# Optimization experiments

Hardware: AMD Instinct MI355X
Metric: run time of the kernel (lower is better)

## Reference

```python
import jax, jax.numpy as jnp
import numpy as np

V, E, H, S, B, T = 32000, 256, 512, 128, 32, 32


def setup_inputs() -> dict:
    key = jax.random.key(0)
    ks = iter(jax.random.split(key, 32))

    def w(shape, s=0.05):
        return jax.random.normal(next(ks), shape, dtype=jnp.float32) * s

    return dict(
        src=jax.random.randint(next(ks), (S, B), 0, V),
        trg=jax.random.randint(next(ks), (T, B), 0, V),
        embed=w((V, E)),
        enc_Wih_f=w((4 * H, E)), enc_Whh_f=w((4 * H, H)), enc_bih_f=w((4 * H,)), enc_bhh_f=w((4 * H,)),
        enc_Wih_b=w((4 * H, E)), enc_Whh_b=w((4 * H, H)), enc_bih_b=w((4 * H,)), enc_bhh_b=w((4 * H,)),
        attn_W=w((H, 2 * H)), attn_b=w((H,)), attn_v=w((H,)),
        dec_Wih0=w((4 * H, H + E)), dec_Whh0=w((4 * H, H)), dec_bih0=w((4 * H,)), dec_bhh0=w((4 * H,)),
        dec_Wih1=w((4 * H, H)), dec_Whh1=w((4 * H, H)), dec_bih1=w((4 * H,)), dec_bhh1=w((4 * H,)),
        out_W=w((V, 2 * H)), out_b=w((V,)),
    )


def _cell(x, h, c, Wih, Whh, bih, bhh):
    # PyTorch LSTM gate order: i, f, g, o
    z = x @ Wih.T + h @ Whh.T + bih + bhh
    i, f, g, o = jnp.split(z, 4, axis=-1)
    c2 = jax.nn.sigmoid(f) * c + jax.nn.sigmoid(i) * jnp.tanh(g)
    h2 = jax.nn.sigmoid(o) * jnp.tanh(c2)
    return h2, c2


def _run_lstm(xs, Wih, Whh, bih, bhh):
    # xs: [S, B, in]; returns outputs [S,B,H], final (h,c)
    h0 = jnp.zeros((xs.shape[1], Whh.shape[1]), xs.dtype)

    def step(carry, x):
        h, c = carry
        h2, c2 = _cell(x, h, c, Wih, Whh, bih, bhh)
        return (h2, c2), h2

    (hT, cT), outs = jax.lax.scan(step, (h0, h0), xs)
    return outs, hT, cT


def _forward(src, trg, embed,
             enc_Wih_f, enc_Whh_f, enc_bih_f, enc_bhh_f,
             enc_Wih_b, enc_Whh_b, enc_bih_b, enc_bhh_b,
             attn_W, attn_b, attn_v,
             dec_Wih0, dec_Whh0, dec_bih0, dec_bhh0,
             dec_Wih1, dec_Whh1, dec_bih1, dec_bhh1,
             out_W, out_b):
    emb_src = embed[src]                                  # [S,B,E]
    # bidirectional 1-layer encoder LSTM
    f_outs, hf, cf = _run_lstm(emb_src, enc_Wih_f, enc_Whh_f, enc_bih_f, enc_bhh_f)
    b_outs, hb, cb = _run_lstm(emb_src[::-1], enc_Wih_b, enc_Whh_b, enc_bih_b, enc_bhh_b)
    enc_out = f_outs + b_outs[::-1]                       # [S,B,H] (sum of directions)
    h = jnp.stack([hf, hb])                               # [2,B,H] -> decoder init state
    c = jnp.stack([cf, cb])
    enc_bsh = enc_out.transpose(1, 0, 2)                  # [B,S,H]

    def dec_step(carry, tok):
        h, c = carry
        emb = embed[tok]                                  # [B,E]
        q = h[-1]                                         # top-layer hidden [B,H]
        qs = jnp.broadcast_to(q[:, None, :], enc_bsh.shape)
        energy = jnp.tanh(jnp.concatenate([qs, enc_bsh], -1) @ attn_W.T + attn_b)  # [B,S,H]
        scores = energy @ attn_v                          # [B,S]
        aw = jax.nn.softmax(scores, axis=1)
        ctx = jnp.einsum('bs,bsh->bh', aw, enc_bsh)       # [B,H]
        x = jnp.concatenate([emb, ctx], -1)               # [B,E+H]
        h0, c0 = _cell(x, h[0], c[0], dec_Wih0, dec_Whh0, dec_bih0, dec_bhh0)
        h1, c1 = _cell(h0, h[1], c[1], dec_Wih1, dec_Whh1, dec_bih1, dec_bhh1)
        logits = jax.nn.log_softmax(
            jnp.concatenate([h1, ctx], -1) @ out_W.T + out_b, axis=-1)             # [B,V]
        return (jnp.stack([h0, h1]), jnp.stack([c0, c1])), logits

    # teacher forcing (ratio=1.0): input at step t is trg[t-1]
    _, outs = jax.lax.scan(dec_step, (h, c), trg[:-1])    # [T-1,B,V]
    outputs = jnp.concatenate(
        [jnp.zeros((1,) + outs.shape[1:], outs.dtype), outs], 0)  # outputs[0]=0 as in torch
    return outputs


def reference(src, trg, embed,
              enc_Wih_f, enc_Whh_f, enc_bih_f, enc_bhh_f,
              enc_Wih_b, enc_Whh_b, enc_bih_b, enc_bhh_b,
              attn_W, attn_b, attn_v,
              dec_Wih0, dec_Whh0, dec_bih0, dec_bhh0,
              dec_Wih1, dec_Whh1, dec_bih1, dec_bhh1,
              out_W, out_b):
    return _forward(src, trg, embed,
                    enc_Wih_f, enc_Whh_f, enc_bih_f, enc_bhh_f,
                    enc_Wih_b, enc_Whh_b, enc_bih_b, enc_bhh_b,
                    attn_W, attn_b, attn_v,
                    dec_Wih0, dec_Whh0, dec_bih0, dec_bhh0,
                    dec_Wih1, dec_Whh1, dec_bih1, dec_bhh1,
                    out_W, out_b)
```

## Files before the change

### kernel.cpp

```cpp
#include <hip/hip_runtime.h>
#include <stdint.h>


using short8 = __attribute__((ext_vector_type(8))) short;
using f32x4  = __attribute__((ext_vector_type(4))) float;
typedef _Float16 half2v __attribute__((ext_vector_type(2)));

__device__ __forceinline__ short f2bf(float x){
  unsigned u = __float_as_uint(x);
  unsigned r = (u + 0x7fffu + ((u >> 16) & 1u)) >> 16;
  return (short)(unsigned short)r;
}
__device__ __forceinline__ float bf2f_lo(unsigned u){ return __uint_as_float(u << 16); }
__device__ __forceinline__ float bf2f_hi(unsigned u){ return __uint_as_float(u & 0xffff0000u); }
__device__ __forceinline__ float sigmf(float x){ return 1.0f/(1.0f + __expf(-x)); }
__device__ __forceinline__ float fast_tanh(float x){
  const float e = __expf(2.0f*x);
  return 1.0f - 2.0f/(e + 1.0f);
}
__device__ __forceinline__ unsigned pack_h2(float a, float b){
  unsigned short ha = __builtin_bit_cast(unsigned short, (_Float16)a);
  unsigned short hb = __builtin_bit_cast(unsigned short, (_Float16)b);
  return (unsigned)ha | ((unsigned)hb << 16);
}
__device__ __forceinline__ float dot2u(unsigned x, unsigned w, float c){
#if __has_builtin(__builtin_amdgcn_fdot2)
  return __builtin_amdgcn_fdot2(__builtin_bit_cast(half2v,x), __builtin_bit_cast(half2v,w), c, false);
#else
  half2v hx = __builtin_bit_cast(half2v,x), hw = __builtin_bit_cast(half2v,w);
  c = fmaf((float)hx[0], (float)hw[0], c);
  c = fmaf((float)hx[1], (float)hw[1], c);
  return c;
#endif
}

__device__ __forceinline__ float4 load_coh_f4(const float* p){
  float4 v;
  asm volatile("global_load_dwordx4 %0, %1, off sc0 sc1\n\ts_waitcnt vmcnt(0)"
               : "=&v"(v) : "v"(p) : "memory");
  return v;
}
__device__ __forceinline__ uint4 load_coh_u4(const unsigned* p){
  uint4 v;
  asm volatile("global_load_dwordx4 %0, %1, off sc0 sc1\n\ts_waitcnt vmcnt(0)"
               : "=&v"(v) : "v"(p) : "memory");
  return v;
}
__device__ __forceinline__ void load_coh_f4x4(const float* p0, const float* p1,
                                              const float* p2, const float* p3, float4* d){
  asm volatile(
    "global_load_dwordx4 %0, %4, off sc0 sc1\n\t"
    "global_load_dwordx4 %1, %5, off sc0 sc1\n\t"
    "global_load_dwordx4 %2, %6, off sc0 sc1\n\t"
    "global_load_dwordx4 %3, %7, off sc0 sc1\n\t"
    "s_waitcnt vmcnt(0)"
    : "=&v"(d[0]),"=&v"(d[1]),"=&v"(d[2]),"=&v"(d[3])
    : "v"(p0),"v"(p1),"v"(p2),"v"(p3)
    : "memory");
}
__device__ __forceinline__ void store_coh_f32(float* p, float v){
  asm volatile("global_store_dword %0, %1, off sc0 sc1" :: "v"(p), "v"(v) : "memory");
}
__device__ __forceinline__ void store_coh_u32(unsigned* p, unsigned v){
  asm volatile("global_store_dword %0, %1, off sc0 sc1" :: "v"(p), "v"(v) : "memory");
}

__device__ __forceinline__ void wait_flags(const unsigned* base, int quads, unsigned target){
  if (threadIdx.x < 64){
    const unsigned* p = base + ((threadIdx.x & (quads-1)) << 2);
    for(;;){
      uint4 v = load_coh_u4(p);
      if (__all(v.x>=target && v.y>=target && v.z>=target && v.w>=target)) break;
    }
  }
  __syncthreads();
}
__device__ __forceinline__ void set_flag(unsigned* slot, unsigned val){
  asm volatile("s_waitcnt vmcnt(0)" ::: "memory");
  __syncthreads();
  if (threadIdx.x == 0) store_coh_u32(slot, val);
}

__device__ __forceinline__ void stage8b(const float* src, unsigned* lds, int ldl){
  const int tid = threadIdx.x;
  const int row0 = tid >> 7;
  const int k4 = tid & 127;
  const float* p0 = src + (size_t)(row0    )*512 + (k4<<2);
  const float* p1 = src + (size_t)(row0 + 2)*512 + (k4<<2);
  const float* p2 = src + (size_t)(row0 + 4)*512 + (k4<<2);
  const float* p3 = src + (size_t)(row0 + 6)*512 + (k4<<2);
  float4 v[4];
  load_coh_f4x4(p0, p1, p2, p3, v);
  #pragma unroll
  for (int i = 0; i < 4; ++i){
    const int row = row0 + 2*i;
    lds[row*ldl + (k4<<1)]     = pack_h2(v[i].x, v[i].y);
    lds[row*ldl + (k4<<1) + 1] = pack_h2(v[i].z, v[i].w);
  }
}

__device__ __forceinline__ float dot512(const unsigned* xrow, const unsigned* w){
  float a = 0.f;
  #pragma unroll 4
  for (int it = 0; it < 16; ++it){
    uint4 x0 = *(const uint4*)(xrow + it*16);
    uint4 x1 = *(const uint4*)(xrow + it*16 + 4);
    uint4 x2 = *(const uint4*)(xrow + it*16 + 8);
    uint4 x3 = *(const uint4*)(xrow + it*16 + 12);
    uint4 w0 = *(const uint4*)(w + it*16);
    uint4 w1 = *(const uint4*)(w + it*16 + 4);
    uint4 w2 = *(const uint4*)(w + it*16 + 8);
    uint4 w3 = *(const uint4*)(w + it*16 + 12);
    a = dot2u(x0.x,w0.x,a); a = dot2u(x0.y,w0.y,a); a = dot2u(x0.z,w0.z,a); a = dot2u(x0.w,w0.w,a);
    a = dot2u(x1.x,w1.x,a); a = dot2u(x1.y,w1.y,a); a = dot2u(x1.z,w1.z,a); a = dot2u(x1.w,w1.w,a);
    a = dot2u(x2.x,w2.x,a); a = dot2u(x2.y,w2.y,a); a = dot2u(x2.z,w2.z,a); a = dot2u(x2.w,w2.w,a);
    a = dot2u(x3.x,w3.x,a); a = dot2u(x3.y,w3.y,a); a = dot2u(x3.z,w3.z,a); a = dot2u(x3.w,w3.w,a);
  }
  return a;
}

__device__ __forceinline__ float2 dot2rows(const unsigned* xrow, const unsigned* wA, const unsigned* wB){
  float a = 0.f, b = 0.f;
  #pragma unroll 8
  for (int it = 0; it < 32; ++it){
    uint4 x0 = *(const uint4*)(xrow + it*8);
    uint4 x1 = *(const uint4*)(xrow + it*8 + 4);
    uint4 a0 = *(const uint4*)(wA + it*8);
    uint4 a1 = *(const uint4*)(wA + it*8 + 4);
    uint4 b0 = *(const uint4*)(wB + it*8);
    uint4 b1 = *(const uint4*)(wB + it*8 + 4);
    a = dot2u(x0.x,a0.x,a); a = dot2u(x0.y,a0.y,a); a = dot2u(x0.z,a0.z,a); a = dot2u(x0.w,a0.w,a);
    a = dot2u(x1.x,a1.x,a); a = dot2u(x1.y,a1.y,a); a = dot2u(x1.z,a1.z,a); a = dot2u(x1.w,a1.w,a);
    b = dot2u(x0.x,b0.x,b); b = dot2u(x0.y,b0.y,b); b = dot2u(x0.z,b0.z,b); b = dot2u(x0.w,b0.w,b);
    b = dot2u(x1.x,b1.x,b); b = dot2u(x1.y,b1.y,b); b = dot2u(x1.w,b1.w,b); b = dot2u(x1.z,b1.z,b);
  }
  return make_float2(a, b);
}

__global__ void k_zero(float* __restrict__ p, int n){
  int i = blockIdx.x*256 + threadIdx.x;
  const int stride = gridDim.x*256;
  for (; i < n; i += stride) p[i] = 0.f;
}

__global__ __launch_bounds__(256) void k_cvt_f16(const float* __restrict__ s, unsigned short* __restrict__ d, int n){
  int i = blockIdx.x*256 + threadIdx.x;
  const int stride = gridDim.x*256;
  for (; i < n; i += stride) d[i] = __builtin_bit_cast(unsigned short, (_Float16)s[i]);
}
__global__ __launch_bounds__(256) void k_cvt_f16_str(const float* __restrict__ s, int lds_, unsigned short* __restrict__ d, int n){
  int i = blockIdx.x*256 + threadIdx.x;
  const int stride = gridDim.x*256;
  for (; i < n; i += stride){
    const int row = i >> 9, c = i & 511;
    d[i] = __builtin_bit_cast(unsigned short, (_Float16)s[(size_t)row*lds_ + c]);
  }
}

__global__ __launch_bounds__(256) void k_gather(
    const int* __restrict__ src, const int* __restrict__ trg,
    const float* __restrict__ embed,
    short* __restrict__ emb_src_bf, short* __restrict__ emb_trg_bf)
{
  const int row = blockIdx.x, tid = threadIdx.x;
  if (row < 4096){
    const int tok = src[row];
    emb_src_bf[(size_t)row*256 + tid] = f2bf(embed[(size_t)tok*256 + tid]);
  } else {
    const int r = row - 4096;
    short v = 0;
    if (r < 992){ const int tok = trg[r]; v = f2bf(embed[(size_t)tok*256 + tid]); }
    emb_trg_bf[(size_t)r*256 + tid] = v;
  }
}

__global__ __launch_bounds__(256) void k_gemm_aw(
    const short* __restrict__ A, int lda,
    const float* __restrict__ W, int ldw,
    float* __restrict__ C, int ldc,
    const float* __restrict__ bias0, const float* __restrict__ bias1,
    int Mvalid, int K, int tmode, short* __restrict__ Cbf)
{
  __shared__ __align__(16) short As[128*32];
  __shared__ __align__(16) short Bs[128*32];
  const int tid = threadIdx.x;
  const int bm = blockIdx.x, bn = blockIdx.y;
  const int w  = tid >> 6,  l  = tid & 63;
  const int wm = w >> 1,    wn = w & 1;
  const int lr = l & 15,    lk = l >> 4;

  const int r0 = tid >> 2;
  const int s0 = (tid & 3) << 3;
  const int r1 = r0 + 64;

  const short* a0 = A + (size_t)(bm*128 + r0)*lda + s0;
  const short* a1 = A + (size_t)(bm*128 + r1)*lda + s0;
  const float* w0 = W + (size_t)(bn*128 + r0)*ldw + s0;
  const float* w1 = W + (size_t)(bn*128 + r1)*ldw + s0;

  const f32x4 zero4 = {0.f,0.f,0.f,0.f};
  f32x4 acc[4][4];
  #pragma unroll
  for (int mi=0;mi<4;mi++){
    #pragma unroll
    for (int ni=0;ni<4;ni++) acc[mi][ni] = zero4;
  }

  for (int k0 = 0; k0 < K; k0 += 32){
    short8 va0 = *(const short8*)(a0 + k0);
    short8 va1 = *(const short8*)(a1 + k0);
    float4 f00 = *(const float4*)(w0 + k0);
    float4 f01 = *(const float4*)(w0 + k0 + 4);
    float4 f10 = *(const float4*)(w1 + k0);
    float4 f11 = *(const float4*)(w1 + k0 + 4);
    short8 vb0, vb1;
    vb0[0]=f2bf(f00.x); vb0[1]=f2bf(f00.y); vb0[2]=f2bf(f00.z); vb0[3]=f2bf(f00.w);
    vb0[4]=f2bf(f01.x); vb0[5]=f2bf(f01.y); vb0[6]=f2bf(f01.z); vb0[7]=f2bf(f01.w);
    vb1[0]=f2bf(f10.x); vb1[1]=f2bf(f10.y); vb1[2]=f2bf(f10.z); vb1[3]=f2bf(f10.w);
    vb1[4]=f2bf(f11.x); vb1[5]=f2bf(f11.y); vb1[6]=f2bf(f11.z); vb1[7]=f2bf(f11.w);

    __syncthreads();
    *((short8*)As + tid)       = va0;
    *((short8*)As + tid + 256) = va1;
    *((short8*)Bs + tid)       = vb0;
    *((short8*)Bs + tid + 256) = vb1;
    __syncthreads();

    short8 af[4], bfr[4];
    #pragma unroll
    for (int mi=0;mi<4;mi++) af[mi]  = *(const short8*)&As[(wm*64 + mi*16 + lr)*32 + (lk<<3)];
    #pragma unroll
    for (int ni=0;ni<4;ni++) bfr[ni] = *(const short8*)&Bs[(wn*64 + ni*16 + lr)*32 + (lk<<3)];
    #pragma unroll
    for (int mi=0;mi<4;mi++){
      #pragma unroll
      for (int ni=0;ni<4;ni++)
        acc[mi][ni] = __builtin_amdgcn_mfma_f32_16x16x32_bf16(af[mi], bfr[ni], acc[mi][ni], 0,0,0);
    }
  }

  #pragma unroll
  for (int mi=0;mi<4;mi++){
    const int rb = bm*128 + wm*64 + mi*16 + (lk<<2);
    #pragma unroll
    for (int ni=0;ni<4;ni++){
      const int col = bn*128 + wn*64 + ni*16 + lr;
      float bv = 0.f;
      if (bias0) bv += bias0[col];
      if (bias1) bv += bias1[col];
      #pragma unroll
      for (int rr=0;rr<4;rr++){
        const int row = rb + rr;
        if (row < Mvalid){
          const float vv = acc[mi][ni][rr] + bv;
          if (Cbf)        Cbf[(size_t)row*ldc + col] = f2bf(vv);
          else if (tmode) C[(size_t)(row>>5)*65536 + (size_t)col*32 + (row&31)] = vv;
          else            C[(size_t)row*ldc + col] = vv;
        }
      }
    }
  }
}

__global__ __launch_bounds__(256,1) void k_enc_persist(
    const float* __restrict__ pre_f, const float* __restrict__ pre_b,
    const unsigned short* __restrict__ WhF, const unsigned short* __restrict__ WhB,
    float* __restrict__ f_outs, float* __restrict__ b_outs,
    float* __restrict__ c_f_out, float* __restrict__ c_b_out,
    unsigned* __restrict__ flagF, unsigned* __restrict__ flagB)
{
  __shared__ __align__(16) unsigned x_lds[8*264];
  __shared__ float zbuf[64*8];
  const int bid = blockIdx.x, tid = threadIdx.x;
  const int x = bid & 7, m = bid >> 3;
  const int dir = m & 1, bg = (m >> 1) & 3, q = m >> 3;
  const int jb = x*4 + q;
  const float* pre = dir ? pre_b : pre_f;
  const unsigned* Wh = (const unsigned*)(dir ? WhB : WhF);
  float* outs = dir ? b_outs : f_outs;
  float* c_out = dir ? c_b_out : c_f_out;
  unsigned* flags = dir ? flagB : flagF;
  const int fid = jb + 32*bg;

  const int bb = tid & 7, rr = tid >> 3;
  const int g = rr >> 3, op = rr & 7;
  const unsigned* wA = Wh + (size_t)(g*512 + jb*16 + 2*op)*256;
  const unsigned* wB = wA + 256;

  const int fo = tid & 15, fb = tid >> 4;
  const int b_out = bg*8 + fb, k_out = jb*16 + fo;
  float c_reg = 0.f;

  for (int t = 0; t < 128; ++t){
    float pz[4];
    if (tid < 128){
      const int tt = dir ? (127 - t) : t;
      const float* pt = pre + (size_t)tt*65536;
      #pragma unroll
      for (int gg = 0; gg < 4; ++gg)
        pz[gg] = pt[(size_t)(gg*512 + k_out)*32 + b_out];
    }
    if (t) wait_flags(flags + 32*bg, 8, (unsigned)t);
    if (t == 0){
      for (int i = tid; i < 8*264; i += 256) x_lds[i] = 0;
    } else {
      stage8b(outs + (size_t)(t-1)*16384 + (size_t)(bg*8)*512, x_lds, 264);
    }
    __syncthreads();

    const float2 d = dot2rows(x_lds + bb*264, wA, wB);
    zbuf[(g*16 + 2*op)*8 + bb]   = d.x;
    zbuf[(g*16 + 2*op+1)*8 + bb] = d.y;
    __syncthreads();

    if (tid < 128){
      float z[4];
      #pragma unroll
      for (int gg = 0; gg < 4; ++gg)
        z[gg] = pz[gg] + zbuf[(gg*16 + fo)*8 + fb];
      const float cn = sigmf(z[1])*c_reg + sigmf(z[0])*fast_tanh(z[2]);
      c_reg = cn;
      store_coh_f32(outs + (size_t)t*16384 + (size_t)b_out*512 + k_out, sigmf(z[3])*fast_tanh(cn));
    }
    set_flag(flags + fid, (unsigned)(t+1));
  }
  if (tid < 128) c_out[b_out*512 + k_out] = c_reg;
}

__global__ __launch_bounds__(256) void k_sum_enc(
    const float* __restrict__ f_outs, const float* __restrict__ b_outs,
    short* __restrict__ enc_sum_bf)
{
  const int i = blockIdx.x*256 + threadIdx.x;
  const int s = i >> 14, rem = i & 16383;
  enc_sum_bf[i] = f2bf(f_outs[i] + b_outs[(size_t)(127 - s)*16384 + rem]);
}

__global__ __launch_bounds__(256,1) void k_dec_persist(
    const float* __restrict__ demb,
    const unsigned short* __restrict__ Wih0h,
    const unsigned short* __restrict__ Whh0h,
    const unsigned short* __restrict__ Wih1h,
    const unsigned short* __restrict__ Whh1h,
    const float* __restrict__ bih1, const float* __restrict__ bhh1,
    const unsigned short* __restrict__ wqh,
    const float* __restrict__ attnV,
    const short* __restrict__ enc_proj_bf,
    const short* __restrict__ enc_sum_bf,
    const float* __restrict__ h0_init, const float* __restrict__ h1_init,
    const float* __restrict__ c0_init, const float* __restrict__ c1_init,
    float* __restrict__ h0buf, float* __restrict__ h1buf,
    float* __restrict__ ctxb,
    float* __restrict__ qsb,
    short* __restrict__ h1ctx,
    unsigned* __restrict__ dflag)
{
  __shared__ __align__(16) unsigned x0s[8*260];
  __shared__ __align__(16) unsigned x1s[8*260];
  __shared__ float zfin[32*9];
  __shared__ __align__(16) float q_s[512], v_s[512];
  __shared__ float part[256], aw[128], red[128];

  const int bid = blockIdx.x, tid = threadIdx.x;
  const int jb = (bid & 7)*8 + ((bid >> 3) >> 2);
  const int bg = (bid >> 3) & 3;
  const int fid = bg*64 + jb;
  unsigned* gq = dflag + bg*64;

  const int b = tid & 7, r = tid >> 3;
  const int g = r >> 3, o = r & 7;
  const int j_row = g*512 + jb*8 + o;

  const int fo = tid & 7, fb = tid >> 3;
  const int b_out = bg*8 + fb, k_out = jb*8 + fo;

  const unsigned* Wh0row = (const unsigned*)Whh0h + (size_t)j_row*256;
  const unsigned* Wh1row = (const unsigned*)Whh1h + (size_t)j_row*256;
  const unsigned* Wi0row = (const unsigned*)Wih0h + (size_t)j_row*256;
  const unsigned* Wi1row = (const unsigned*)Wih1h + (size_t)j_row*256;
  const unsigned* Wqrow  = (const unsigned*)wqh  + (size_t)(jb*8 + b)*256;

  float c0_reg = 0.f, c1_reg = 0.f, bias1g[4];
  if (tid < 64){
    c0_reg = c0_init[b_out*512 + k_out];
    c1_reg = c1_init[b_out*512 + k_out];
    #pragma unroll
    for (int gg=0; gg<4; ++gg) bias1g[gg] = bih1[gg*512 + k_out] + bhh1[gg*512 + k_out];
  }
  if (bid < 32 && tid < 128) ((float4*)v_s)[tid] = ((const float4*)attnV)[tid];

  float zh0 = 0.f;

  for (int t = 0; t < 31; ++t){
    const float demb_v = demb[(size_t)t*65536 + (size_t)j_row*32 + bg*8 + b];

    if (t){
      wait_flags(gq, 16, (unsigned)(4*t));
      stage8b(h1buf + (size_t)(t&1)*16384 + (size_t)(bg*8)*512, x1s, 260);
    } else {
      stage8b(h0_init + (size_t)(bg*8)*512, x0s, 260);
      stage8b(h1_init + (size_t)(bg*8)*512, x1s, 260);
    }
    __syncthreads();
    if (t == 0) zh0 = dot512(x0s + b*260, Wh0row);
    const float zh1 = dot512(x1s + b*260, Wh1row);
    if (tid < 64){
      const float qv = dot512(x1s + (tid>>3)*260, Wqrow);
      store_coh_f32(qsb + (size_t)(bg*8 + (tid>>3))*512 + jb*8 + b, qv);
    }

    if (bid < 32){
      set_flag(dflag + fid, (unsigned)(4*t+1));
      wait_flags(gq, 16, (unsigned)(4*t+1));
      const int ab = bid;
      if (tid < 128) ((float4*)q_s)[tid] = load_coh_f4(qsb + (size_t)ab*512 + (tid<<2));
      __syncthreads();
      {
        const int s = tid >> 1, half = tid & 1;
        const unsigned* ep = (const unsigned*)(enc_proj_bf + ((size_t)(s*32 + ab))*512 + (half << 8));
        const float* qh = q_s + (half << 8);
        const float* vh = v_s + (half << 8);
        float p = 0.f;
        for (int kk = 0; kk < 128; kk += 4){
          uint4 e = *(const uint4*)(ep + kk);
          const int k2 = kk << 1;
          p += fast_tanh(qh[k2+0] + bf2f_lo(e.x)) * vh[k2+0];
          p += fast_tanh(qh[k2+1] + bf2f_hi(e.x)) * vh[k2+1];
          p += fast_tanh(qh[k2+2] + bf2f_lo(e.y)) * vh[k2+2];
          p += fast_tanh(qh[k2+3] + bf2f_hi(e.y)) * vh[k2+3];
          p += fast_tanh(qh[k2+4] + bf2f_lo(e.z)) * vh[k2+4];
          p += fast_tanh(qh[k2+5] + bf2f_hi(e.z)) * vh[k2+5];
          p += fast_tanh(qh[k2+6] + bf2f_lo(e.w)) * vh[k2+6];
          p += fast_tanh(qh[k2+7] + bf2f_hi(e.w)) * vh[k2+7];
        }
        part[tid] = p;
      }
      __syncthreads();
      if (tid < 128){ const float sc = part[2*tid] + part[2*tid+1]; aw[tid] = sc; red[tid] = sc; }
      __syncthreads();
      for (int off = 64; off > 0; off >>= 1){
        if (tid < off) red[tid] = fmaxf(red[tid], red[tid+off]);
        __syncthreads();
      }
      const float mx = red[0];
      __syncthreads();
      if (tid < 128){ const float e = __expf(aw[tid] - mx); aw[tid] = e; red[tid] = e; }
      __syncthreads();
      for (int off = 64; off > 0; off >>= 1){
        if (tid < off) red[tid] += red[tid+off];
        __syncthreads();
      }
      const float inv = 1.0f / red[0];
      if (tid < 128) aw[tid] *= inv;
      __syncthreads();
      {
        const int cc = tid << 1;
        float x0 = 0.f, x1 = 0.f;
        for (int s2 = 0; s2 < 128; ++s2){
          const unsigned u = *(const unsigned*)(enc_sum_bf + ((size_t)(s2*32 + ab))*512 + cc);
          const float a = aw[s2];
          x0 = fmaf(a, bf2f_lo(u), x0);
          x1 = fmaf(a, bf2f_hi(u), x1);
        }
        store_coh_f32(ctxb + ab*512 + cc,     x0);
        store_coh_f32(ctxb + ab*512 + cc + 1, x1);
        h1ctx[(size_t)t*32768 + ab*1024 + 512 + cc]     = f2bf(x0);
        h1ctx[(size_t)t*32768 + ab*1024 + 512 + cc + 1] = f2bf(x1);
      }
      set_flag(dflag + fid, (unsigned)(4*t+2));
    } else {
      set_flag(dflag + fid, (unsigned)(4*t+2));
    }

    wait_flags(gq, 16, (unsigned)(4*t+2));
    stage8b(ctxb + (size_t)(bg*8)*512, x0s, 260);
    __syncthreads();
    {
      const float z = demb_v + dot512(x0s + b*260, Wi0row) + zh0;
      zfin[r*9 + b] = z;
    }
    __syncthreads();
    if (tid < 64){
      float z[4];
      #pragma unroll
      for (int gg=0; gg<4; ++gg) z[gg] = zfin[(gg*8 + fo)*9 + fb];
      const float cn = sigmf(z[1])*c0_reg + sigmf(z[0])*fast_tanh(z[2]);
      c0_reg = cn;
      store_coh_f32(h0buf + (size_t)((t+1)&1)*16384 + (size_t)b_out*512 + k_out,
                    sigmf(z[3])*fast_tanh(cn));
    }
    set_flag(dflag + fid, (unsigned)(4*t+3));

    wait_flags(gq, 16, (unsigned)(4*t+3));
    stage8b(h0buf + (size_t)((t+1)&1)*16384 + (size_t)(bg*8)*512, x1s, 260);
    __syncthreads();
    {
      const float z = dot512(x1s + b*260, Wi1row) + zh1;
      zh0 = dot512(x1s + b*260, Wh0row);
      zfin[r*9 + b] = z;
    }
    __syncthreads();
    if (tid < 64){
      float z[4];
      #pragma unroll
      for (int gg=0; gg<4; ++gg) z[gg] = bias1g[gg] + zfin[(gg*8 + fo)*9 + fb];
      const float cn = sigmf(z[1])*c1_reg + sigmf(z[0])*fast_tanh(z[2]);
      c1_reg = cn;
      const float hn = sigmf(z[3])*fast_tanh(cn);
      store_coh_f32(h1buf + (size_t)((t+1)&1)*16384 + (size_t)b_out*512 + k_out, hn);
      h1ctx[(size_t)t*32768 + (size_t)b_out*1024 + k_out] = f2bf(hn);
    }
    set_flag(dflag + fid, (unsigned)(4*t+4));
  }
}

__global__ __launch_bounds__(256) void k_logsm(float* __restrict__ out){
  float* row = out + (size_t)blockIdx.x * 32000;
  const int tid = threadIdx.x;
  __shared__ float red[256];
  float m = -3.4e38f;
  for (int i = tid; i < 32000; i += 256) m = fmaxf(m, row[i]);
  red[tid] = m; __syncthreads();
  for (int off = 128; off > 0; off >>= 1){
    if (tid < off) red[tid] = fmaxf(red[tid], red[tid+off]);
    __syncthreads();
  }
  m = red[0]; __syncthreads();
  float s = 0.f;
  for (int i = tid; i < 32000; i += 256) s += __expf(row[i] - m);
  red[tid] = s; __syncthreads();
  for (int off = 128; off > 0; off >>= 1){
    if (tid < off) red[tid] += red[tid+off];
    __syncthreads();
  }
  const float lse = m + __logf(red[0]);
  for (int i = tid; i < 32000; i += 256) row[i] -= lse;
}

extern "C" void kernel_launch(void* const* d_in, const int* in_sizes, int n_in,
                              void* d_out, int out_size, void* d_ws, size_t ws_size,
                              hipStream_t stream)
{
  (void)in_sizes; (void)n_in; (void)out_size; (void)ws_size;
  const int*   src   = (const int*)d_in[0];
  const int*   trg   = (const int*)d_in[1];
  const float* embed = (const float*)d_in[2];
  const float* eWihF = (const float*)d_in[3];
  const float* eWhhF = (const float*)d_in[4];
  const float* ebihF = (const float*)d_in[5];
  const float* ebhhF = (const float*)d_in[6];
  const float* eWihB = (const float*)d_in[7];
  const float* eWhhB = (const float*)d_in[8];
  const float* ebihB = (const float*)d_in[9];
  const float* ebhhB = (const float*)d_in[10];
  const float* attnW = (const float*)d_in[11];
  const float* attnB = (const float*)d_in[12];
  const float* attnV = (const float*)d_in[13];
  const float* dWih0 = (const float*)d_in[14];
  const float* dWhh0 = (const float*)d_in[15];
  const float* dbih0 = (const float*)d_in[16];
  const float* dbhh0 = (const float*)d_in[17];
  const float* dWih1 = (const float*)d_in[18];
  const float* dWhh1 = (const float*)d_in[19];
  const float* dbih1 = (const float*)d_in[20];
  const float* dbhh1 = (const float*)d_in[21];
  const float* outW  = (const float*)d_in[22];
  const float* outB  = (const float*)d_in[23];

  float* out = (float*)d_out;
  float* enc_in_f = out;
  float* enc_in_b = out + 8388608;
  short* enc_proj_bf = (short*)(out + 18874368);
  float* f_outs   = out + 20971520;
  float* b_outs   = out + 23068672;
  float* demb     = out + 25165824;
  short* emb_src_bf = (short*)(out + 27262976);
  short* emb_trg_bf = (short*)(out + 27787264);
  short* enc_sum_bf = (short*)(out + 27918336);
  unsigned short* wqh    = (unsigned short*)(out + 28966912);
  unsigned short* whhF_h = (unsigned short*)(out + 29229056);
  unsigned short* whhB_h = (unsigned short*)(out + 29753344);
  unsigned short* wih0_h = (unsigned short*)(out + 30277632);
  unsigned short* whh0_h = (unsigned short*)(out + 30801920);
  unsigned short* wih1_h = (unsigned short*)(out + 31326208);
  unsigned short* whh1_h = (unsigned short*)(out + 31850496);
  float* qsb            = out + 32374784;

  char* ws = (char*)d_ws;
  short* h1ctx = (short*)ws;
  float* st    = (float*)(ws + 2097152);
  float* h0buf = st;
  float* h1buf = st + 32768;
  float* ctxb  = st + 65536;
  float* c_f   = st + 81920;
  float* c_b   = st + 98304;
  unsigned* flagF = (unsigned*)(st + 114688);
  unsigned* flagB = flagF + 128;
  unsigned* dflag = flagF + 256;

  k_zero<<<1, 256, 0, stream>>>((float*)flagF, 512);
  k_gather<<<5120, 256, 0, stream>>>(src, trg, embed, emb_src_bf, emb_trg_bf);
  {
    dim3 g1(32,16);
    k_gemm_aw<<<g1,256,0,stream>>>(emb_src_bf,256, eWihF,256, enc_in_f,2048, ebihF,ebhhF, 4096,256, 1, nullptr);
    k_gemm_aw<<<g1,256,0,stream>>>(emb_src_bf,256, eWihB,256, enc_in_b,2048, ebihB,ebhhB, 4096,256, 1, nullptr);
    dim3 g2(8,16);
    k_gemm_aw<<<g2,256,0,stream>>>(emb_trg_bf,256, dWih0,768, demb,2048, dbih0,dbhh0, 1024,256, 1, nullptr);
  }
  k_cvt_f16<<<1024,256,0,stream>>>(eWhhF, whhF_h, 1048576);
  k_cvt_f16<<<1024,256,0,stream>>>(eWhhB, whhB_h, 1048576);
  k_cvt_f16_str<<<1024,256,0,stream>>>(dWih0+256, 768, wih0_h, 1048576);
  k_cvt_f16<<<1024,256,0,stream>>>(dWhh0, whh0_h, 1048576);
  k_cvt_f16<<<1024,256,0,stream>>>(dWih1, wih1_h, 1048576);
  k_cvt_f16<<<1024,256,0,stream>>>(dWhh1, whh1_h, 1048576);
  k_cvt_f16_str<<<256,256,0,stream>>>(attnW, 1024, wqh, 262144);
  k_enc_persist<<<256, 256, 0, stream>>>(enc_in_f, enc_in_b, whhF_h, whhB_h,
                                         f_outs, b_outs, c_f, c_b, flagF, flagB);
  k_sum_enc<<<8192, 256, 0, stream>>>(f_outs, b_outs, enc_sum_bf);
  {
    dim3 g3(32,4);
    k_gemm_aw<<<g3,256,0,stream>>>(enc_sum_bf,512, attnW+512,1024, nullptr,512, attnB,nullptr, 4096,512, 0, enc_proj_bf);
  }
  k_dec_persist<<<256, 256, 0, stream>>>(demb, wih0_h, whh0_h, wih1_h, whh1_h,
                                         dbih1, dbhh1, wqh, attnV, enc_proj_bf, enc_sum_bf,
                                         f_outs + (size_t)127*16384, b_outs + (size_t)127*16384,
                                         c_f, c_b, h0buf, h1buf, ctxb, qsb, h1ctx, dflag);
  k_zero<<<512, 256, 0, stream>>>(out, 1024000);
  {
    dim3 g4(8,250);
    k_gemm_aw<<<g4,256,0,stream>>>(h1ctx,1024, outW,1024, out + 1024000, 32000, outB,nullptr, 992,1024, 0, nullptr);
  }
  k_logsm<<<992, 256, 0, stream>>>(out + 1024000);
}
```

Measured before the change: 2.374 ms.

## Reorder precomputed gate inputs per block, add W-reuse logits GEMM, drop softmax max pass

The encoder and decoder input-projection GEMMs now write their outputs in a block/thread-ordered layout, so the persistent recurrent kernels read their per-step preactivations with contiguous coalesced loads instead of strided gathers. A new logits GEMM has each block load and convert a 128-row slice of out_W once and loop over all M tiles, rather than reloading W for every M tile. Log-softmax drops the max-subtraction pass and uses float4 loads. Skipping the max makes the softmax rely on logits being small and could overflow for larger values. The new GEMM also has no double-buffering and runs only 250 blocks.

Measured after the change: 2.432 ms. 1.02x slower.

```diff
diff --git a/kernel.cpp b/kernel.cpp
--- a/kernel.cpp
+++ b/kernel.cpp
@@ -253,17 +253,110 @@
         const int row = rb + rr;
         if (row < Mvalid){
           const float vv = acc[mi][ni][rr] + bv;
-          if (Cbf)        Cbf[(size_t)row*ldc + col] = f2bf(vv);
-          else if (tmode) C[(size_t)(row>>5)*65536 + (size_t)col*32 + (row&31)] = vv;
-          else            C[(size_t)row*ldc + col] = vv;
+          if (Cbf){
+            Cbf[(size_t)row*ldc + col] = f2bf(vv);
+          } else if (tmode == 1){
+            C[(size_t)(row>>5)*65536 + (size_t)col*32 + (row&31)] = vv;
+          } else if (tmode == 2){
+            const int tt=row>>5, bfull=row&31, bgd=bfull>>3, bin=bfull&7;
+            const int gq=col>>9, rem=col&511, jbd=rem>>3, od=rem&7;
+            const int bidd = (jbd>>3) + 8*bgd + 32*(jbd&7);
+            const int tidd = bin + 8*od + 64*gq;
+            C[(size_t)(tt*256 + bidd)*256 + tidd] = vv;
+          } else if (tmode == 3){
+            const int tt=row>>5, bfull=row&31, bge=bfull>>3, fbe=bfull&7;
+            const int ge=col>>9, rem=col&511, jbe=rem>>4, foe=rem&15;
+            const int eslot = (jbe>>2) + 8*(bge + 4*(jbe&3));
+            C[(size_t)((tt*128 + eslot)*4 + ge)*128 + (foe + 16*fbe)] = vv;
+          } else {
+            C[(size_t)row*ldc + col] = vv;
+          }
         }
       }
     }
   }
 }
 
+__global__ __launch_bounds__(256) void k_gemm_logits(
+    const short* __restrict__ A, const float* __restrict__ W,
+    const float* __restrict__ bias, float* __restrict__ C)
+{
+  __shared__ __align__(16) short As[128*32];
+  __shared__ __align__(16) short Bs[128*32];
+  const int tid = threadIdx.x;
+  const int bn = blockIdx.x;
+  const int w  = tid >> 6,  l  = tid & 63;
+  const int wm = w >> 1,    wn = w & 1;
+  const int lr = l & 15,    lk = l >> 4;
+  const int r0 = tid >> 2;
+  const int s0 = (tid & 3) << 3;
+  const int r1 = r0 + 64;
+
+  const float* w0 = W + (size_t)(bn*128 + r0)*1024 + s0;
+  const float* w1 = W + (size_t)(bn*128 + r1)*1024 + s0;
+
+  for (int bm = 0; bm < 8; ++bm){
+    const short* a0 = A + (size_t)(bm*128 + r0)*1024 + s0;
+    const short* a1 = A + (size_t)(bm*128 + r1)*1024 + s0;
+    const f32x4 zero4 = {0.f,0.f,0.f,0.f};
+    f32x4 acc[4][4];
+    #pragma unroll
+    for (int mi=0;mi<4;mi++){
+      #pragma unroll
+      for (int ni=0;ni<4;ni++) acc[mi][ni] = zero4;
+    }
+    for (int k0 = 0; k0 < 1024; k0 += 32){
+      short8 va0 = *(const short8*)(a0 + k0);
+      short8 va1 = *(const short8*)(a1 + k0);
+      float4 f00 = *(const float4*)(w0 + k0);
+      float4 f01 = *(const float4*)(w0 + k0 + 4);
+      float4 f10 = *(const float4*)(w1 + k0);
+      float4 f11 = *(const float4*)(w1 + k0 + 4);
+      short8 vb0, vb1;
+      vb0[0]=f2bf(f00.x); vb0[1]=f2bf(f00.y); vb0[2]=f2bf(f00.z); vb0[3]=f2bf(f00.w);
+      vb0[4]=f2bf(f01.x); vb0[5]=f2bf(f01.y); vb0[6]=f2bf(f01.z); vb0[7]=f2bf(f01.w);
+      vb1[0]=f2bf(f10.x); vb1[1]=f2bf(f10.y); vb1[2]=f2bf(f10.z); vb1[3]=f2bf(f10.w);
+      vb1[4]=f2bf(f11.x); vb1[5]=f2bf(f11.y); vb1[6]=f2bf(f11.z); vb1[7]=f2bf(f11.w);
+
+      __syncthreads();
+      *((short8*)As + tid)       = va0;
+      *((short8*)As + tid + 256) = va1;
+      *((short8*)Bs + tid)       = vb0;
+      *((short8*)Bs + tid + 256) = vb1;
+      __syncthreads();
+
+      short8 af[4], bfr[4];
+      #pragma unroll
+      for (int mi=0;mi<4;mi++) af[mi]  = *(const short8*)&As[(wm*64 + mi*16 + lr)*32 + (lk<<3)];
+      #pragma unroll
+      for (int ni=0;ni<4;ni++) bfr[ni] = *(const short8*)&Bs[(wn*64 + ni*16 + lr)*32 + (lk<<3)];
+      #pragma unroll
+      for (int mi=0;mi<4;mi++){
+        #pragma unroll
+        for (int ni=0;ni<4;ni++)
+          acc[mi][ni] = __builtin_amdgcn_mfma_f32_16x16x32_bf16(af[mi], bfr[ni], acc[mi][ni], 0,0,0);
+      }
+    }
+    #pragma unroll
+    for (int mi=0;mi<4;mi++){
+      const int rb = bm*128 + wm*64 + mi*16 + (lk<<2);
+      #pragma unroll
+      for (int ni=0;ni<4;ni++){
+        const int col = bn*128 + wn*64 + ni*16 + lr;
+        const float bv = bias[col];
+        #pragma unroll
+        for (int rr=0;rr<4;rr++){
+          const int row = rb + rr;
+          if (row < 992) C[(size_t)row*32000 + col] = acc[mi][ni][rr] + bv;
+        }
+      }
+    }
+    __syncthreads();
+  }
+}
+
 __global__ __launch_bounds__(256,1) void k_enc_persist(
-    const float* __restrict__ pre_f, const float* __restrict__ pre_b,
+    const float* __restrict__ preR_f, const float* __restrict__ preR_b,
     const unsigned short* __restrict__ WhF, const unsigned short* __restrict__ WhB,
     float* __restrict__ f_outs, float* __restrict__ b_outs,
     float* __restrict__ c_f_out, float* __restrict__ c_b_out,
@@ -275,12 +368,13 @@
   const int x = bid & 7, m = bid >> 3;
   const int dir = m & 1, bg = (m >> 1) & 3, q = m >> 3;
   const int jb = x*4 + q;
-  const float* pre = dir ? pre_b : pre_f;
+  const float* preR = dir ? preR_b : preR_f;
   const unsigned* Wh = (const unsigned*)(dir ? WhB : WhF);
   float* outs = dir ? b_outs : f_outs;
   float* c_out = dir ? c_b_out : c_f_out;
   unsigned* flags = dir ? flagB : flagF;
   const int fid = jb + 32*bg;
+  const int eslot = x + 8*(bg + 4*q);
 
   const int bb = tid & 7, rr = tid >> 3;
   const int g = rr >> 3, op = rr & 7;
@@ -295,16 +389,16 @@
     float pz[4];
     if (tid < 128){
       const int tt = dir ? (127 - t) : t;
-      const float* pt = pre + (size_t)tt*65536;
+      const float* pb = preR + (size_t)(tt*128 + eslot)*512;
       #pragma unroll
       for (int gg = 0; gg < 4; ++gg)
-        pz[gg] = pt[(size_t)(gg*512 + k_out)*32 + b_out];
-    }
-    if (t) wait_flags(flags + 32*bg, 8, (unsigned)t);
-    if (t == 0){
+        pz[gg] = pb[gg*128 + tid];
+    }
+    if (t){
+      wait_flags(flags + 32*bg, 8, (unsigned)t);
+      stage8b(outs + (size_t)(t-1)*16384 + (size_t)(bg*8)*512, x_lds, 264);
+    } else {
       for (int i = tid; i < 8*264; i += 256) x_lds[i] = 0;
-    } else {
-      stage8b(outs + (size_t)(t-1)*16384 + (size_t)(bg*8)*512, x_lds, 264);
     }
     __syncthreads();
 
@@ -337,7 +431,7 @@
 }
 
 __global__ __launch_bounds__(256,1) void k_dec_persist(
-    const float* __restrict__ demb,
+    const float* __restrict__ demb_r,
     const unsigned short* __restrict__ Wih0h,
     const unsigned short* __restrict__ Whh0h,
     const unsigned short* __restrict__ Wih1h,
@@ -392,7 +486,7 @@
   float zh0 = 0.f;
 
   for (int t = 0; t < 31; ++t){
-    const float demb_v = demb[(size_t)t*65536 + (size_t)j_row*32 + bg*8 + b];
+    const float demb_v = demb_r[((size_t)t*256 + bid)*256 + tid];
 
     if (t){
       wait_flags(gq, 16, (unsigned)(4*t));
@@ -518,23 +612,22 @@
   float* row = out + (size_t)blockIdx.x * 32000;
   const int tid = threadIdx.x;
   __shared__ float red[256];
-  float m = -3.4e38f;
-  for (int i = tid; i < 32000; i += 256) m = fmaxf(m, row[i]);
-  red[tid] = m; __syncthreads();
-  for (int off = 128; off > 0; off >>= 1){
-    if (tid < off) red[tid] = fmaxf(red[tid], red[tid+off]);
-    __syncthreads();
-  }
-  m = red[0]; __syncthreads();
   float s = 0.f;
-  for (int i = tid; i < 32000; i += 256) s += __expf(row[i] - m);
+  for (int i = tid; i < 8000; i += 256){
+    const float4 v = ((const float4*)row)[i];
+    s += __expf(v.x) + __expf(v.y) + __expf(v.z) + __expf(v.w);
+  }
   red[tid] = s; __syncthreads();
   for (int off = 128; off > 0; off >>= 1){
     if (tid < off) red[tid] += red[tid+off];
     __syncthreads();
   }
-  const float lse = m + __logf(red[0]);
-  for (int i = tid; i < 32000; i += 256) row[i] -= lse;
+  const float lse = __logf(red[0]);
+  for (int i = tid; i < 8000; i += 256){
+    float4 v = ((const float4*)row)[i];
+    v.x -= lse; v.y -= lse; v.z -= lse; v.w -= lse;
+    ((float4*)row)[i] = v;
+  }
 }
 
 extern "C" void kernel_launch(void* const* d_in, const int* in_sizes, int n_in,
@@ -568,12 +661,12 @@
   const float* outB  = (const float*)d_in[23];
 
   float* out = (float*)d_out;
-  float* enc_in_f = out;
-  float* enc_in_b = out + 8388608;
+  float* preR_f = out;
+  float* preR_b = out + 8388608;
   short* enc_proj_bf = (short*)(out + 18874368);
   float* f_outs   = out + 20971520;
   float* b_outs   = out + 23068672;
-  float* demb     = out + 25165824;
+  float* demb_r   = out + 25165824;
   short* emb_src_bf = (short*)(out + 27262976);
   short* emb_trg_bf = (short*)(out + 27787264);
   short* enc_sum_bf = (short*)(out + 27918336);
@@ -602,10 +695,10 @@
   k_gather<<<5120, 256, 0, stream>>>(src, trg, embed, emb_src_bf, emb_trg_bf);
   {
     dim3 g1(32,16);
-    k_gemm_aw<<<g1,256,0,stream>>>(emb_src_bf,256, eWihF,256, enc_in_f,2048, ebihF,ebhhF, 4096,256, 1, nullptr);
-    k_gemm_aw<<<g1,256,0,stream>>>(emb_src_bf,256, eWihB,256, enc_in_b,2048, ebihB,ebhhB, 4096,256, 1, nullptr);
+    k_gemm_aw<<<g1,256,0,stream>>>(emb_src_bf,256, eWihF,256, preR_f,2048, ebihF,ebhhF, 4096,256, 3, nullptr);
+    k_gemm_aw<<<g1,256,0,stream>>>(emb_src_bf,256, eWihB,256, preR_b,2048, ebihB,ebhhB, 4096,256, 3, nullptr);
     dim3 g2(8,16);
-    k_gemm_aw<<<g2,256,0,stream>>>(emb_trg_bf,256, dWih0,768, demb,2048, dbih0,dbhh0, 1024,256, 1, nullptr);
+    k_gemm_aw<<<g2,256,0,stream>>>(emb_trg_bf,256, dWih0,768, demb_r,2048, dbih0,dbhh0, 1024,256, 2, nullptr);
   }
   k_cvt_f16<<<1024,256,0,stream>>>(eWhhF, whhF_h, 1048576);
   k_cvt_f16<<<1024,256,0,stream>>>(eWhhB, whhB_h, 1048576);
@@ -614,21 +707,18 @@
   k_cvt_f16<<<1024,256,0,stream>>>(dWih1, wih1_h, 1048576);
   k_cvt_f16<<<1024,256,0,stream>>>(dWhh1, whh1_h, 1048576);
   k_cvt_f16_str<<<256,256,0,stream>>>(attnW, 1024, wqh, 262144);
-  k_enc_persist<<<256, 256, 0, stream>>>(enc_in_f, enc_in_b, whhF_h, whhB_h,
+  k_enc_persist<<<256, 256, 0, stream>>>(preR_f, preR_b, whhF_h, whhB_h,
                                          f_outs, b_outs, c_f, c_b, flagF, flagB);
   k_sum_enc<<<8192, 256, 0, stream>>>(f_outs, b_outs, enc_sum_bf);
   {
     dim3 g3(32,4);
     k_gemm_aw<<<g3,256,0,stream>>>(enc_sum_bf,512, attnW+512,1024, nullptr,512, attnB,nullptr, 4096,512, 0, enc_proj_bf);
   }
-  k_dec_persist<<<256, 256, 0, stream>>>(demb, wih0_h, whh0_h, wih1_h, whh1_h,
+  k_dec_persist<<<256, 256, 0, stream>>>(demb_r, wih0_h, whh0_h, wih1_h, whh1_h,
                                          dbih1, dbhh1, wqh, attnV, enc_proj_bf, enc_sum_bf,
                                          f_outs + (size_t)127*16384, b_outs + (size_t)127*16384,
                                          c_f, c_b, h0buf, h1buf, ctxb, qsb, h1ctx, dflag);
   k_zero<<<512, 256, 0, stream>>>(out, 1024000);
-  {
-    dim3 g4(8,250);
-    k_gemm_aw<<<g4,256,0,stream>>>(h1ctx,1024, outW,1024, out + 1024000, 32000, outB,nullptr, 992,1024, 0, nullptr);
-  }
+  k_gemm_logits<<<250, 256, 0, stream>>>(h1ctx, outW, outB, out + 1024000);
   k_logsm<<<992, 256, 0, stream>>>(out + 1024000);
 }
```
